# Kernel tuning notes

Measured on AMD Instinct MI355X. Metric: run time of the kernel, lower is better.

Reference implementation:

```python
import jax, jax.numpy as jnp
import numpy as np

N = 100_000      # nodes
E = 1_600_000    # edges (avg degree 16)
D_IN = 128
D_H = 128
D_P = 128
D_OUT = 64


def setup_inputs() -> dict:
    key = jax.random.key(0)
    ks = jax.random.split(key, 10)
    x = jax.random.normal(ks[0], (N, D_IN), dtype=jnp.float32)
    edge_index = jax.random.randint(ks[1], (2, E), 0, N, dtype=jnp.int64)
    # Mix_Pass layer 0: Linear(in->hidden, bias=False) + separate bias (zero-init)
    W1 = jax.random.normal(ks[2], (D_H, D_IN), dtype=jnp.float32) * 0.05
    b1 = jnp.zeros((D_H,), dtype=jnp.float32)
    # Mix_Pass layer 1: hidden->hidden
    W2 = jax.random.normal(ks[3], (D_H, D_H), dtype=jnp.float32) * 0.05
    b2 = jnp.zeros((D_H,), dtype=jnp.float32)
    # projection MLP
    fcW1 = jax.random.normal(ks[4], (D_P, D_H), dtype=jnp.float32) * 0.05
    fcb1 = jnp.zeros((D_P,), dtype=jnp.float32)
    fcW2 = jax.random.normal(ks[5], (D_OUT, D_P), dtype=jnp.float32) * 0.05
    fcb2 = jnp.zeros((D_OUT,), dtype=jnp.float32)
    return dict(x=x, edge_index=edge_index, W1=W1, b1=b1, W2=W2, b2=b2,
                fcW1=fcW1, fcb1=fcb1, fcW2=fcW2, fcb2=fcb2)


def _gcn_norm_with_self_loops(edge_index, n_nodes):
    # add_self_loops then gcn_norm (sym, improved=False, loops already added)
    loop = jnp.arange(n_nodes, dtype=edge_index.dtype)
    row = jnp.concatenate([edge_index[0], loop])  # source
    col = jnp.concatenate([edge_index[1], loop])  # target
    ew = jnp.ones(row.shape[0], dtype=jnp.float32)
    deg = jax.ops.segment_sum(ew, col, num_segments=n_nodes)
    dinv = jnp.where(deg > 0, jax.lax.rsqrt(deg), 0.0)
    return row, col, dinv[row] * ew * dinv[col]


def _mix_pass(z, W, b, row, col, ew, n_nodes):
    z = z @ W.T                                   # [N, out]
    msg = ew[:, None] * z[row]                    # gather source feats, scale
    out = jax.ops.segment_sum(msg, col, num_segments=n_nodes)  # scatter-add
    return out + b


def reference(x, edge_index, W1, b1, W2, b2, fcW1, fcb1, fcW2, fcb2):
    n_nodes = x.shape[0]
    row, col, ew = _gcn_norm_with_self_loops(edge_index, n_nodes)
    # dropout is identity in eval mode
    z = jax.nn.relu(_mix_pass(x, W1, b1, row, col, ew, n_nodes))
    zs = _mix_pass(z, W2, b2, row, col, ew, n_nodes)
    # project: elu(fc1) -> log_softmax(fc2)
    h = jax.nn.elu(zs @ fcW1.T + fcb1)
    res = jax.nn.log_softmax(h @ fcW2.T + fcb2, axis=1)
    return zs, res
```

## Files before the change

kernel.cpp:

```cpp
#include <hip/hip_runtime.h>
#include <hip/hip_bf16.h>

typedef __bf16 bf16_t;
typedef bf16_t bf16x8 __attribute__((ext_vector_type(8)));
typedef bf16_t bf16x4 __attribute__((ext_vector_type(4)));
typedef bf16_t bf16x2 __attribute__((ext_vector_type(2)));
typedef float f32x4 __attribute__((ext_vector_type(4)));

#define DEG_CAP 64
#define BKT_SHIFT 8
#define BKT_CAP 6144
#define EPT 8

__device__ __forceinline__ void cvt4(const float* __restrict__ s, bf16_t* __restrict__ d, int i) {
    f32x4 v = ((const f32x4*)s)[i];
    bf16x4 o;
#pragma unroll
    for (int j = 0; j < 4; ++j) o[j] = (bf16_t)v[j];
    ((bf16x4*)d)[i] = o;
}

__global__ void setup_k(const float* xf, bf16_t* Xbf, int nx4,
                        const float* W1f, bf16_t* W1b,
                        const float* W2f, bf16_t* W2b,
                        const float* fW1f, bf16_t* fW1b,
                        const float* fW2f, bf16_t* fW2b,
                        int* gbcnt, int NB, int* yzero) {
    int i = blockIdx.x * blockDim.x + threadIdx.x;
    if (i < nx4) { cvt4(xf, Xbf, i); return; }
    i -= nx4;
    if (i < 4096) { cvt4(W1f, W1b, i); return; }
    i -= 4096;
    if (i < 4096) { cvt4(W2f, W2b, i); return; }
    i -= 4096;
    if (i < 4096) { cvt4(fW1f, fW1b, i); return; }
    i -= 4096;
    if (i < 2048) { cvt4(fW2f, fW2b, i); return; }
    i -= 2048;
    if (i < NB) { gbcnt[i] = 0; return; }
    i -= NB;
    if (i < 64) yzero[i] = 0;
}

__global__ __launch_bounds__(256) void bucket_scatter_k(const int* __restrict__ ei,
                                                        int* __restrict__ gbcnt,
                                                        unsigned* __restrict__ grec,
                                                        int E, int N) {
    __shared__ int hist[512];
    __shared__ int base[512];
    const int tid = threadIdx.x;
    const int NB = (N + 255) >> BKT_SHIFT;
    for (int i = tid; i < NB; i += 256) hist[i] = 0;
    __syncthreads();

    const int wave = tid >> 6, lane = tid & 63;
    const long e0 = (long)blockIdx.x * (256 * EPT) + (long)wave * (64 * EPT) + lane;
    const bool i64 = (ei[1] == 0) & (ei[3] == 0) & (ei[5] == 0) & (ei[7] == 0);

    unsigned rec[EPT];
    int lof[EPT];
    int bk[EPT];
#pragma unroll
    for (int j = 0; j < EPT; ++j) {
        long e = e0 + (long)j * 64;
        bk[j] = -1;
        if (e < E) {
            int r, c;
            if (i64) { r = ei[2 * e]; c = ei[2 * (long)E + 2 * e]; }
            else     { r = ei[e];     c = ei[(long)E + e]; }
            r = ((unsigned)r < (unsigned)N) ? r : 0;
            c = ((unsigned)c < (unsigned)N) ? c : 0;
            int b = c >> BKT_SHIFT;
            rec[j] = ((unsigned)r << BKT_SHIFT) | (unsigned)(c & 255);
            bk[j] = b;
            lof[j] = atomicAdd(&hist[b], 1);
        }
    }
    __syncthreads();
    for (int i = tid; i < NB; i += 256)
        base[i] = hist[i] ? atomicAdd(&gbcnt[i], hist[i]) : 0;
    __syncthreads();
#pragma unroll
    for (int j = 0; j < EPT; ++j) {
        if (bk[j] >= 0) {
            int pos = base[bk[j]] + lof[j];
            if (pos < BKT_CAP)
                grec[(size_t)bk[j] * BKT_CAP + pos] = rec[j];
        }
    }
}

__global__ __launch_bounds__(256) void bucket_place_k(const int* __restrict__ gbcnt,
                                                      const unsigned* __restrict__ grec,
                                                      int* __restrict__ cnt,
                                                      int* __restrict__ srcx, int N) {
    __shared__ int lcnt[256];
    const int b = blockIdx.x, tid = threadIdx.x;
    lcnt[tid] = 0;
    __syncthreads();
    int ne = gbcnt[b];
    if (ne > BKT_CAP) ne = BKT_CAP;
    const unsigned* rp = grec + (size_t)b * BKT_CAP;
    const int node0 = b << BKT_SHIFT;
    for (int i = tid; i < ne; i += 256) {
        unsigned rec = rp[i];
        int cl = rec & 255;
        int r  = rec >> BKT_SHIFT;
        int p = atomicAdd(&lcnt[cl], 1);
        if (p < DEG_CAP) srcx[(size_t)(node0 + cl) * DEG_CAP + p] = r;
    }
    __syncthreads();
    int node = node0 + tid;
    if (node < N) cnt[node] = lcnt[tid];
}

template <int RELU, int WF32>
__global__ __launch_bounds__(256) void gather_k(const bf16_t* __restrict__ Y,
                                                const int* __restrict__ cnt,
                                                const int* __restrict__ srcx,
                                                const float* __restrict__ bias,
                                                bf16_t* __restrict__ out,
                                                float* __restrict__ out2, int n) {
    int node = blockIdx.x * 4 + (threadIdx.x >> 6);
    if (node >= n) return;
    int lane = threadIdx.x & 63;
    int l16 = lane & 15;
    int quad = lane >> 4;
    int c = cnt[node];
    float di = rsqrtf((float)c + 1.0f);
    int cg = (c < DEG_CAP) ? c : DEG_CAP;
    const int* sl = srcx + (size_t)node * DEG_CAP;
    const bf16_t* Yl = Y + l16 * 8;

    bf16x8 ys = *(const bf16x8*)(Yl + (size_t)node * 128);

    float acc[8];
#pragma unroll
    for (int j = 0; j < 8; ++j) acc[j] = 0.f;

    for (int e = 0; e < cg; e += 16) {
        int4 sq = *(const int4*)(sl + e + quad * 4);
        int idx0 = e + quad * 4;
        int s0 = (idx0 + 0 < cg) ? sq.x : n;
        int s1 = (idx0 + 1 < cg) ? sq.y : n;
        int s2 = (idx0 + 2 < cg) ? sq.z : n;
        int s3 = (idx0 + 3 < cg) ? sq.w : n;
        bf16x8 y0 = *(const bf16x8*)(Yl + (size_t)s0 * 128);
        bf16x8 y1 = *(const bf16x8*)(Yl + (size_t)s1 * 128);
        bf16x8 y2 = *(const bf16x8*)(Yl + (size_t)s2 * 128);
        bf16x8 y3 = *(const bf16x8*)(Yl + (size_t)s3 * 128);
#pragma unroll
        for (int j = 0; j < 8; ++j)
            acc[j] += (float)y0[j] + (float)y1[j] + (float)y2[j] + (float)y3[j];
    }

#pragma unroll
    for (int j = 0; j < 8; ++j) {
        acc[j] += __shfl_xor(acc[j], 16);
        acc[j] += __shfl_xor(acc[j], 32);
    }

    f32x4 b0 = ((const f32x4*)bias)[l16 * 2];
    f32x4 b1 = ((const f32x4*)bias)[l16 * 2 + 1];
    float v[8];
#pragma unroll
    for (int j = 0; j < 8; ++j) {
        float bb = (j < 4) ? b0[j & 3] : b1[j & 3];
        v[j] = di * ((float)ys[j] + acc[j]) + bb;
        if (RELU) v[j] = fmaxf(v[j], 0.f);
    }

    if (quad == 0) {
        bf16x8 o;
#pragma unroll
        for (int j = 0; j < 8; ++j) o[j] = (bf16_t)v[j];
        *(bf16x8*)(out + (size_t)node * 128 + l16 * 8) = o;
    }
    if (WF32) {
        if (quad == 1) {
            f32x4 w = {v[0], v[1], v[2], v[3]};
            *(f32x4*)(out2 + (size_t)node * 128 + l16 * 8) = w;
        } else if (quad == 2) {
            f32x4 w = {v[4], v[5], v[6], v[7]};
            *(f32x4*)(out2 + (size_t)node * 128 + l16 * 8 + 4) = w;
        }
    }
}

template <int OC, int MODE, int MT>
__global__ __launch_bounds__(256) void gemm_k(const bf16_t* __restrict__ A,
                                              const bf16_t* __restrict__ W,
                                              const float* __restrict__ bias,
                                              const int* __restrict__ cnt,
                                              bf16_t* __restrict__ out,
                                              float* __restrict__ outf, int nrows) {
    const int lane = threadIdx.x & 63;
    const int wave = threadIdx.x >> 6;
    const int l16 = lane & 15;
    const int quad = lane >> 4;
    constexpr int NT = OC / 16;
    const int ntiles = (nrows + 15) >> 4;
    const int t0 = (blockIdx.x * 4 + wave) * MT;
    if (t0 >= ntiles) return;

    f32x4 acc[MT][NT];
#pragma unroll
    for (int mt = 0; mt < MT; ++mt)
#pragma unroll
        for (int n = 0; n < NT; ++n) acc[mt][n] = (f32x4){0.f, 0.f, 0.f, 0.f};

    const bf16_t* arow[MT];
#pragma unroll
    for (int mt = 0; mt < MT; ++mt) {
        int r = t0 * 16 + mt * 16 + l16;
        if (r > nrows - 1) r = nrows - 1;
        arow[mt] = A + (size_t)r * 128 + quad * 8;
    }
    const bf16_t* wrow = W + (size_t)l16 * 128 + quad * 8;

#pragma unroll
    for (int kt = 0; kt < 4; ++kt) {
        bf16x8 a[MT];
#pragma unroll
        for (int mt = 0; mt < MT; ++mt) a[mt] = *(const bf16x8*)(arow[mt] + kt * 32);
#pragma unroll
        for (int n = 0; n < NT; ++n) {
            bf16x8 b = *(const bf16x8*)(wrow + (size_t)n * 2048 + kt * 32);
#pragma unroll
            for (int mt = 0; mt < MT; ++mt)
                acc[mt][n] = __builtin_amdgcn_mfma_f32_16x16x32_bf16(a[mt], b, acc[mt][n], 0, 0, 0);
        }
    }

#pragma unroll
    for (int mt = 0; mt < MT; ++mt) {
        int m0 = (t0 + mt) * 16;
        if (m0 >= nrows) break;
        if constexpr (MODE == 0) {
#pragma unroll
            for (int r = 0; r < 4; ++r) {
                int row = m0 + quad * 4 + r;
                if (row < nrows) {
                    float sc = rsqrtf((float)cnt[row] + 1.0f);
#pragma unroll
                    for (int n = 0; n < NT; ++n)
                        out[(size_t)row * OC + n * 16 + l16] = (bf16_t)(sc * acc[mt][n][r]);
                }
            }
        } else if constexpr (MODE == 1) {
#pragma unroll
            for (int n = 0; n < NT; ++n) {
                float bb = bias[n * 16 + l16];
#pragma unroll
                for (int r = 0; r < 4; ++r) {
                    int row = m0 + quad * 4 + r;
                    float v = acc[mt][n][r] + bb;
                    v = (v > 0.0f) ? v : (expf(v) - 1.0f);
                    if (row < nrows)
                        out[(size_t)row * OC + n * 16 + l16] = (bf16_t)v;
                }
            }
        } else {
#pragma unroll
            for (int r = 0; r < 4; ++r) {
                float v[NT];
#pragma unroll
                for (int n = 0; n < NT; ++n) v[n] = acc[mt][n][r] + bias[n * 16 + l16];
                float mx = v[0];
#pragma unroll
                for (int n = 1; n < NT; ++n) mx = fmaxf(mx, v[n]);
#pragma unroll
                for (int m = 8; m >= 1; m >>= 1) mx = fmaxf(mx, __shfl_xor(mx, m));
                float s = 0.0f;
#pragma unroll
                for (int n = 0; n < NT; ++n) s += expf(v[n] - mx);
#pragma unroll
                for (int m = 8; m >= 1; m >>= 1) s += __shfl_xor(s, m);
                float lse = mx + logf(s);
                int row = m0 + quad * 4 + r;
                if (row < nrows)
#pragma unroll
                    for (int n = 0; n < NT; ++n)
                        outf[(size_t)row * OC + n * 16 + l16] = v[n] - lse;
            }
        }
    }
}

extern "C" void kernel_launch(void* const* d_in, const int* in_sizes, int n_in,
                              void* d_out, int out_size, void* d_ws, size_t ws_size,
                              hipStream_t stream) {
    const float* xf    = (const float*)d_in[0];
    const int*   ei    = (const int*)d_in[1];
    const float* W1f   = (const float*)d_in[2];
    const float* b1f   = (const float*)d_in[3];
    const float* W2f   = (const float*)d_in[4];
    const float* b2f   = (const float*)d_in[5];
    const float* fcW1f = (const float*)d_in[6];
    const float* fcb1f = (const float*)d_in[7];
    const float* fcW2f = (const float*)d_in[8];
    const float* fcb2f = (const float*)d_in[9];

    const int N = in_sizes[0] / 128;
    const int E = in_sizes[1] / 2;
    const int NB = (N + 255) >> BKT_SHIFT;

    float* zs_out  = (float*)d_out;
    float* res_out = (float*)d_out + (size_t)N * 128;

    char* ws = (char*)d_ws;
    size_t o = 0;
    auto carve = [&](size_t bytes) { void* p = ws + o; o = (o + bytes + 255) & ~255UL; return p; };
    int*      cnt   = (int*)carve((size_t)N * 4);
    int*      srcx  = (int*)carve((size_t)N * DEG_CAP * 4);
    bf16_t*   Xbf   = (bf16_t*)carve((size_t)N * 128 * 2);
    bf16_t*   Ybf   = (bf16_t*)carve((size_t)(N + 1) * 128 * 2);
    bf16_t*   W1b   = (bf16_t*)carve(128 * 128 * 2);
    bf16_t*   W2b   = (bf16_t*)carve(128 * 128 * 2);
    bf16_t*   fW1b  = (bf16_t*)carve(128 * 128 * 2);
    bf16_t*   fW2b  = (bf16_t*)carve(64 * 128 * 2);
    unsigned* grec  = (unsigned*)carve((size_t)NB * BKT_CAP * 4);
    int*      gbcnt = (int*)carve((size_t)NB * 4);

    const int B = 256;
    const int ntiles = (N + 15) / 16;
    const int gblocks = (ntiles + 15) / 16;
    const int nodeblocks = (N + 3) / 4;
    const int nx4 = N * 32;
    const int nsetup = nx4 + 4096 * 3 + 2048 + NB + 64;
    const int ablocks = (E + 256 * EPT - 1) / (256 * EPT);

    setup_k<<<(nsetup + B - 1) / B, B, 0, stream>>>(xf, Xbf, nx4, W1f, W1b, W2f, W2b,
                                                    fcW1f, fW1b, fcW2f, fW2b, gbcnt, NB,
                                                    (int*)(Ybf + (size_t)N * 128));
    bucket_scatter_k<<<ablocks, B, 0, stream>>>(ei, gbcnt, grec, E, N);
    bucket_place_k<<<NB, B, 0, stream>>>(gbcnt, grec, cnt, srcx, N);

    gemm_k<128, 0, 4><<<gblocks, B, 0, stream>>>(Xbf, W1b, nullptr, cnt, Ybf, nullptr, N);
    gather_k<1, 0><<<nodeblocks, B, 0, stream>>>(Ybf, cnt, srcx, b1f, Xbf, nullptr, N);

    gemm_k<128, 0, 4><<<gblocks, B, 0, stream>>>(Xbf, W2b, nullptr, cnt, Ybf, nullptr, N);
    gather_k<0, 1><<<nodeblocks, B, 0, stream>>>(Ybf, cnt, srcx, b2f, Xbf, zs_out, N);

    gemm_k<128, 1, 4><<<gblocks, B, 0, stream>>>(Xbf, fW1b, fcb1f, nullptr, Ybf, nullptr, N);
    gemm_k<64, 2, 4><<<gblocks, B, 0, stream>>>(Ybf, fW2b, fcb2f, nullptr, nullptr, res_out, N);
}
```

Before: 414.4 us.

## Fuse projection MLP into one head kernel and gather two nodes per wave

Replaces the two projection GEMM launches with a single head kernel. It keeps the ELU hidden tile in LDS and runs the second MFMA GEMM plus log_softmax there, so the intermediate never goes through global memory. The gather kernel now processes two nodes per wave to raise memory-level parallelism. bucket_place pads neighbour lists with the dummy node index so the per-lane bounds masks can be dropped. It also switches edge indexing to 32-bit and lowers the GEMM MT tile from 4 to 2 for more blocks. Costs are higher register pressure in the gather and extra padding writes.

```diff
diff --git a/kernel.cpp b/kernel.cpp
--- a/kernel.cpp
+++ b/kernel.cpp
@@ -54,7 +54,7 @@
     __syncthreads();
 
     const int wave = tid >> 6, lane = tid & 63;
-    const long e0 = (long)blockIdx.x * (256 * EPT) + (long)wave * (64 * EPT) + lane;
+    const int e0 = blockIdx.x * (256 * EPT) + wave * (64 * EPT) + lane;
     const bool i64 = (ei[1] == 0) & (ei[3] == 0) & (ei[5] == 0) & (ei[7] == 0);
 
     unsigned rec[EPT];
@@ -62,12 +62,12 @@
     int bk[EPT];
 #pragma unroll
     for (int j = 0; j < EPT; ++j) {
-        long e = e0 + (long)j * 64;
+        int e = e0 + j * 64;
         bk[j] = -1;
         if (e < E) {
             int r, c;
-            if (i64) { r = ei[2 * e]; c = ei[2 * (long)E + 2 * e]; }
-            else     { r = ei[e];     c = ei[(long)E + e]; }
+            if (i64) { r = ei[2 * e]; c = ei[2 * E + 2 * e]; }
+            else     { r = ei[e];     c = ei[E + e]; }
             r = ((unsigned)r < (unsigned)N) ? r : 0;
             c = ((unsigned)c < (unsigned)N) ? c : 0;
             int b = c >> BKT_SHIFT;
@@ -111,7 +111,15 @@
     }
     __syncthreads();
     int node = node0 + tid;
-    if (node < N) cnt[node] = lcnt[tid];
+    if (node < N) {
+        int c = lcnt[tid];
+        cnt[node] = c;
+        int cc = (c < DEG_CAP) ? c : DEG_CAP;
+        int pe = (cc + 15) & ~15;
+        if (pe > DEG_CAP) pe = DEG_CAP;
+        int* s = srcx + (size_t)node * DEG_CAP;
+        for (int p = cc; p < pe; ++p) s[p] = N;
+    }
 }
 
 template <int RELU, int WF32>
@@ -121,68 +129,104 @@
                                                 const float* __restrict__ bias,
                                                 bf16_t* __restrict__ out,
                                                 float* __restrict__ out2, int n) {
-    int node = blockIdx.x * 4 + (threadIdx.x >> 6);
-    if (node >= n) return;
-    int lane = threadIdx.x & 63;
-    int l16 = lane & 15;
-    int quad = lane >> 4;
-    int c = cnt[node];
-    float di = rsqrtf((float)c + 1.0f);
-    int cg = (c < DEG_CAP) ? c : DEG_CAP;
-    const int* sl = srcx + (size_t)node * DEG_CAP;
+    int node0 = (blockIdx.x * 4 + (threadIdx.x >> 6)) * 2;
+    if (node0 >= n) return;
+    const int lane = threadIdx.x & 63;
+    const int l16 = lane & 15;
+    const int quad = lane >> 4;
+    const bool has1 = node0 + 1 < n;
+    const int node1 = has1 ? node0 + 1 : n;
+
+    int2 cc = *(const int2*)(cnt + node0);
+    int c0 = cc.x;
+    int c1 = has1 ? cc.y : 0;
+    float di0 = rsqrtf((float)c0 + 1.0f);
+    float di1 = rsqrtf((float)c1 + 1.0f);
+    int cg0 = (c0 < DEG_CAP) ? c0 : DEG_CAP;
+    int cg1 = (c1 < DEG_CAP) ? c1 : DEG_CAP;
+    int nb0 = (cg0 + 15) & ~15;
+    int nb1 = (cg1 + 15) & ~15;
+    int nbm = nb0 > nb1 ? nb0 : nb1;
+
+    const int* sl0 = srcx + (size_t)node0 * DEG_CAP;
+    const int* sl1 = srcx + (size_t)node1 * DEG_CAP;
     const bf16_t* Yl = Y + l16 * 8;
 
-    bf16x8 ys = *(const bf16x8*)(Yl + (size_t)node * 128);
-
-    float acc[8];
-#pragma unroll
-    for (int j = 0; j < 8; ++j) acc[j] = 0.f;
-
-    for (int e = 0; e < cg; e += 16) {
-        int4 sq = *(const int4*)(sl + e + quad * 4);
-        int idx0 = e + quad * 4;
-        int s0 = (idx0 + 0 < cg) ? sq.x : n;
-        int s1 = (idx0 + 1 < cg) ? sq.y : n;
-        int s2 = (idx0 + 2 < cg) ? sq.z : n;
-        int s3 = (idx0 + 3 < cg) ? sq.w : n;
-        bf16x8 y0 = *(const bf16x8*)(Yl + (size_t)s0 * 128);
-        bf16x8 y1 = *(const bf16x8*)(Yl + (size_t)s1 * 128);
-        bf16x8 y2 = *(const bf16x8*)(Yl + (size_t)s2 * 128);
-        bf16x8 y3 = *(const bf16x8*)(Yl + (size_t)s3 * 128);
-#pragma unroll
-        for (int j = 0; j < 8; ++j)
-            acc[j] += (float)y0[j] + (float)y1[j] + (float)y2[j] + (float)y3[j];
+    bf16x8 ys0 = *(const bf16x8*)(Yl + (size_t)node0 * 128);
+    bf16x8 ys1 = *(const bf16x8*)(Yl + (size_t)node1 * 128);
+
+    float acc0[8], acc1[8];
+#pragma unroll
+    for (int j = 0; j < 8; ++j) { acc0[j] = 0.f; acc1[j] = 0.f; }
+
+    for (int e = 0; e < nbm; e += 16) {
+        int4 sq0, sq1;
+        bool d0 = e < nb0, d1 = e < nb1;
+        if (d0) sq0 = *(const int4*)(sl0 + e + quad * 4);
+        if (d1) sq1 = *(const int4*)(sl1 + e + quad * 4);
+        if (d0) {
+            bf16x8 y0 = *(const bf16x8*)(Yl + (size_t)sq0.x * 128);
+            bf16x8 y1 = *(const bf16x8*)(Yl + (size_t)sq0.y * 128);
+            bf16x8 y2 = *(const bf16x8*)(Yl + (size_t)sq0.z * 128);
+            bf16x8 y3 = *(const bf16x8*)(Yl + (size_t)sq0.w * 128);
+#pragma unroll
+            for (int j = 0; j < 8; ++j)
+                acc0[j] += (float)y0[j] + (float)y1[j] + (float)y2[j] + (float)y3[j];
+        }
+        if (d1) {
+            bf16x8 y0 = *(const bf16x8*)(Yl + (size_t)sq1.x * 128);
+            bf16x8 y1 = *(const bf16x8*)(Yl + (size_t)sq1.y * 128);
+            bf16x8 y2 = *(const bf16x8*)(Yl + (size_t)sq1.z * 128);
+            bf16x8 y3 = *(const bf16x8*)(Yl + (size_t)sq1.w * 128);
+#pragma unroll
+            for (int j = 0; j < 8; ++j)
+                acc1[j] += (float)y0[j] + (float)y1[j] + (float)y2[j] + (float)y3[j];
+        }
     }
 
 #pragma unroll
     for (int j = 0; j < 8; ++j) {
-        acc[j] += __shfl_xor(acc[j], 16);
-        acc[j] += __shfl_xor(acc[j], 32);
+        acc0[j] += __shfl_xor(acc0[j], 16);
+        acc0[j] += __shfl_xor(acc0[j], 32);
+        acc1[j] += __shfl_xor(acc1[j], 16);
+        acc1[j] += __shfl_xor(acc1[j], 32);
     }
 
     f32x4 b0 = ((const f32x4*)bias)[l16 * 2];
     f32x4 b1 = ((const f32x4*)bias)[l16 * 2 + 1];
-    float v[8];
+    float v0[8], v1[8];
 #pragma unroll
     for (int j = 0; j < 8; ++j) {
         float bb = (j < 4) ? b0[j & 3] : b1[j & 3];
-        v[j] = di * ((float)ys[j] + acc[j]) + bb;
-        if (RELU) v[j] = fmaxf(v[j], 0.f);
+        v0[j] = di0 * ((float)ys0[j] + acc0[j]) + bb;
+        v1[j] = di1 * ((float)ys1[j] + acc1[j]) + bb;
+        if (RELU) { v0[j] = fmaxf(v0[j], 0.f); v1[j] = fmaxf(v1[j], 0.f); }
     }
 
     if (quad == 0) {
         bf16x8 o;
 #pragma unroll
-        for (int j = 0; j < 8; ++j) o[j] = (bf16_t)v[j];
-        *(bf16x8*)(out + (size_t)node * 128 + l16 * 8) = o;
+        for (int j = 0; j < 8; ++j) o[j] = (bf16_t)v0[j];
+        *(bf16x8*)(out + (size_t)node0 * 128 + l16 * 8) = o;
+    } else if (quad == 1 && has1) {
+        bf16x8 o;
+#pragma unroll
+        for (int j = 0; j < 8; ++j) o[j] = (bf16_t)v1[j];
+        *(bf16x8*)(out + (size_t)node1 * 128 + l16 * 8) = o;
     }
     if (WF32) {
-        if (quad == 1) {
-            f32x4 w = {v[0], v[1], v[2], v[3]};
-            *(f32x4*)(out2 + (size_t)node * 128 + l16 * 8) = w;
-        } else if (quad == 2) {
-            f32x4 w = {v[4], v[5], v[6], v[7]};
-            *(f32x4*)(out2 + (size_t)node * 128 + l16 * 8 + 4) = w;
+        if (quad == 2) {
+            f32x4 w = {v0[0], v0[1], v0[2], v0[3]};
+            *(f32x4*)(out2 + (size_t)node0 * 128 + l16 * 8) = w;
+        } else if (quad == 3) {
+            f32x4 w = {v0[4], v0[5], v0[6], v0[7]};
+            *(f32x4*)(out2 + (size_t)node0 * 128 + l16 * 8 + 4) = w;
+        } else if (quad == 0 && has1) {
+            f32x4 w = {v1[0], v1[1], v1[2], v1[3]};
+            *(f32x4*)(out2 + (size_t)node1 * 128 + l16 * 8) = w;
+        } else if (quad == 1 && has1) {
+            f32x4 w = {v1[4], v1[5], v1[6], v1[7]};
+            *(f32x4*)(out2 + (size_t)node1 * 128 + l16 * 8 + 4) = w;
         }
     }
 }
@@ -236,54 +280,101 @@
     for (int mt = 0; mt < MT; ++mt) {
         int m0 = (t0 + mt) * 16;
         if (m0 >= nrows) break;
-        if constexpr (MODE == 0) {
-#pragma unroll
-            for (int r = 0; r < 4; ++r) {
-                int row = m0 + quad * 4 + r;
-                if (row < nrows) {
-                    float sc = rsqrtf((float)cnt[row] + 1.0f);
-#pragma unroll
-                    for (int n = 0; n < NT; ++n)
-                        out[(size_t)row * OC + n * 16 + l16] = (bf16_t)(sc * acc[mt][n][r]);
-                }
+#pragma unroll
+        for (int r = 0; r < 4; ++r) {
+            int row = m0 + quad * 4 + r;
+            if (row < nrows) {
+                float sc = rsqrtf((float)cnt[row] + 1.0f);
+#pragma unroll
+                for (int n = 0; n < NT; ++n)
+                    out[(size_t)row * OC + n * 16 + l16] = (bf16_t)(sc * acc[mt][n][r]);
             }
-        } else if constexpr (MODE == 1) {
-#pragma unroll
-            for (int n = 0; n < NT; ++n) {
-                float bb = bias[n * 16 + l16];
-#pragma unroll
-                for (int r = 0; r < 4; ++r) {
-                    int row = m0 + quad * 4 + r;
-                    float v = acc[mt][n][r] + bb;
-                    v = (v > 0.0f) ? v : (expf(v) - 1.0f);
-                    if (row < nrows)
-                        out[(size_t)row * OC + n * 16 + l16] = (bf16_t)v;
-                }
-            }
-        } else {
-#pragma unroll
-            for (int r = 0; r < 4; ++r) {
-                float v[NT];
-#pragma unroll
-                for (int n = 0; n < NT; ++n) v[n] = acc[mt][n][r] + bias[n * 16 + l16];
-                float mx = v[0];
-#pragma unroll
-                for (int n = 1; n < NT; ++n) mx = fmaxf(mx, v[n]);
-#pragma unroll
-                for (int m = 8; m >= 1; m >>= 1) mx = fmaxf(mx, __shfl_xor(mx, m));
-                float s = 0.0f;
-#pragma unroll
-                for (int n = 0; n < NT; ++n) s += expf(v[n] - mx);
-#pragma unroll
-                for (int m = 8; m >= 1; m >>= 1) s += __shfl_xor(s, m);
-                float lse = mx + logf(s);
-                int row = m0 + quad * 4 + r;
-                if (row < nrows)
-#pragma unroll
-                    for (int n = 0; n < NT; ++n)
-                        outf[(size_t)row * OC + n * 16 + l16] = v[n] - lse;
-            }
-        }
+        }
+    }
+}
+
+#define LDW 136
+__global__ __launch_bounds__(256) void head_k(const bf16_t* __restrict__ A,
+                                              const bf16_t* __restrict__ W1,
+                                              const float* __restrict__ b1,
+                                              const bf16_t* __restrict__ W2,
+                                              const float* __restrict__ b2,
+                                              float* __restrict__ outf, int nrows) {
+    __shared__ bf16_t hl[4][16 * LDW];
+    const int lane = threadIdx.x & 63;
+    const int wave = threadIdx.x >> 6;
+    const int l16 = lane & 15;
+    const int quad = lane >> 4;
+    const int ntiles = (nrows + 15) >> 4;
+    int t = blockIdx.x * 4 + wave;
+    const bool live = t < ntiles;
+    if (!live) t = ntiles - 1;
+    const int m0 = t * 16;
+
+    f32x4 acc[8];
+#pragma unroll
+    for (int n = 0; n < 8; ++n) acc[n] = (f32x4){0.f, 0.f, 0.f, 0.f};
+    int r0 = m0 + l16;
+    if (r0 > nrows - 1) r0 = nrows - 1;
+    const bf16_t* arow = A + (size_t)r0 * 128 + quad * 8;
+    const bf16_t* wrow = W1 + (size_t)l16 * 128 + quad * 8;
+#pragma unroll
+    for (int kt = 0; kt < 4; ++kt) {
+        bf16x8 a = *(const bf16x8*)(arow + kt * 32);
+#pragma unroll
+        for (int n = 0; n < 8; ++n) {
+            bf16x8 b = *(const bf16x8*)(wrow + (size_t)n * 2048 + kt * 32);
+            acc[n] = __builtin_amdgcn_mfma_f32_16x16x32_bf16(a, b, acc[n], 0, 0, 0);
+        }
+    }
+    bf16_t* hw = hl[wave];
+#pragma unroll
+    for (int n = 0; n < 8; ++n) {
+        float bb = b1[n * 16 + l16];
+#pragma unroll
+        for (int r = 0; r < 4; ++r) {
+            float v = acc[n][r] + bb;
+            v = (v > 0.0f) ? v : (expf(v) - 1.0f);
+            hw[(quad * 4 + r) * LDW + n * 16 + l16] = (bf16_t)v;
+        }
+    }
+    __syncthreads();
+
+    f32x4 acc2[4];
+#pragma unroll
+    for (int n = 0; n < 4; ++n) acc2[n] = (f32x4){0.f, 0.f, 0.f, 0.f};
+    const bf16_t* hrow = hw + l16 * LDW + quad * 8;
+    const bf16_t* wrow2 = W2 + (size_t)l16 * 128 + quad * 8;
+#pragma unroll
+    for (int kt = 0; kt < 4; ++kt) {
+        bf16x8 a = *(const bf16x8*)(hrow + kt * 32);
+#pragma unroll
+        for (int n = 0; n < 4; ++n) {
+            bf16x8 b = *(const bf16x8*)(wrow2 + (size_t)n * 2048 + kt * 32);
+            acc2[n] = __builtin_amdgcn_mfma_f32_16x16x32_bf16(a, b, acc2[n], 0, 0, 0);
+        }
+    }
+#pragma unroll
+    for (int r = 0; r < 4; ++r) {
+        float v[4];
+#pragma unroll
+        for (int n = 0; n < 4; ++n) v[n] = acc2[n][r] + b2[n * 16 + l16];
+        float mx = v[0];
+#pragma unroll
+        for (int n = 1; n < 4; ++n) mx = fmaxf(mx, v[n]);
+#pragma unroll
+        for (int m = 8; m >= 1; m >>= 1) mx = fmaxf(mx, __shfl_xor(mx, m));
+        float s = 0.0f;
+#pragma unroll
+        for (int n = 0; n < 4; ++n) s += expf(v[n] - mx);
+#pragma unroll
+        for (int m = 8; m >= 1; m >>= 1) s += __shfl_xor(s, m);
+        float lse = mx + logf(s);
+        int row = m0 + quad * 4 + r;
+        if (live && row < nrows)
+#pragma unroll
+            for (int n = 0; n < 4; ++n)
+                outf[(size_t)row * 64 + n * 16 + l16] = v[n] - lse;
     }
 }
 
@@ -324,8 +415,9 @@
 
     const int B = 256;
     const int ntiles = (N + 15) / 16;
-    const int gblocks = (ntiles + 15) / 16;
-    const int nodeblocks = (N + 3) / 4;
+    const int gblocks = (ntiles + 7) / 8;
+    const int hblocks = (ntiles + 3) / 4;
+    const int nodeblocks = (N + 7) / 8;
     const int nx4 = N * 32;
     const int nsetup = nx4 + 4096 * 3 + 2048 + NB + 64;
     const int ablocks = (E + 256 * EPT - 1) / (256 * EPT);
@@ -336,12 +428,11 @@
     bucket_scatter_k<<<ablocks, B, 0, stream>>>(ei, gbcnt, grec, E, N);
     bucket_place_k<<<NB, B, 0, stream>>>(gbcnt, grec, cnt, srcx, N);
 
-    gemm_k<128, 0, 4><<<gblocks, B, 0, stream>>>(Xbf, W1b, nullptr, cnt, Ybf, nullptr, N);
+    gemm_k<128, 0, 2><<<gblocks, B, 0, stream>>>(Xbf, W1b, nullptr, cnt, Ybf, nullptr, N);
     gather_k<1, 0><<<nodeblocks, B, 0, stream>>>(Ybf, cnt, srcx, b1f, Xbf, nullptr, N);
 
-    gemm_k<128, 0, 4><<<gblocks, B, 0, stream>>>(Xbf, W2b, nullptr, cnt, Ybf, nullptr, N);
+    gemm_k<128, 0, 2><<<gblocks, B, 0, stream>>>(Xbf, W2b, nullptr, cnt, Ybf, nullptr, N);
     gather_k<0, 1><<<nodeblocks, B, 0, stream>>>(Ybf, cnt, srcx, b2f, Xbf, zs_out, N);
 
-    gemm_k<128, 1, 4><<<gblocks, B, 0, stream>>>(Xbf, fW1b, fcb1f, nullptr, Ybf, nullptr, N);
-    gemm_k<64, 2, 4><<<gblocks, B, 0, stream>>>(Ybf, fW2b, fcb2f, nullptr, nullptr, res_out, N);
-}
+    head_k<<<hblocks, B, 0, stream>>>(Xbf, fW1b, fcb1f, fW2b, fcb2f, res_out, N);
+}
```

Result: no change. 417.2 us (+0.7%).
